# Performance work log

Hardware: AMD Instinct MI355X
Metric: run time of the kernel (lower is better)

## Reference

```python
import jax, jax.numpy as jnp
import numpy as np

N_ROW = 50000
N_COL = 50000
E = 600000
D = 128
NEG_SLOPE = 0.01  # torch LeakyReLU default


def _leaky(x):
    return jnp.where(x >= 0, x, NEG_SLOPE * x)


def _mlp(x, W1, b1, W2, b2):
    # (Linear -> LeakyReLU) x2, matching nn.Sequential in Conv_layer
    h = _leaky(x @ W1 + b1)
    return _leaky(h @ W2 + b2)


def setup_inputs() -> dict:
    key = jax.random.key(0)
    ks = jax.random.split(key, 16)
    inp = {
        "feat_row": jax.random.normal(ks[0], (N_ROW, D), jnp.float32),
        "feat_col": jax.random.normal(ks[1], (N_COL, D), jnp.float32),
        "src_c2r": jax.random.randint(ks[2], (E,), 0, N_COL, jnp.int32),
        "dst_c2r": jax.random.randint(ks[3], (E,), 0, N_ROW, jnp.int32),
        "w_c2r": jax.random.uniform(ks[4], (E,), jnp.float32),
        "src_r2c": jax.random.randint(ks[5], (E,), 0, N_ROW, jnp.int32),
        "dst_r2c": jax.random.randint(ks[6], (E,), 0, N_COL, jnp.int32),
        "w_r2c": jax.random.uniform(ks[7], (E,), jnp.float32),
        "W1_c2r": jax.random.normal(ks[8], (D, D), jnp.float32) / np.sqrt(D),
        "b1_c2r": jax.random.normal(ks[9], (D,), jnp.float32) * 0.01,
        "W2_c2r": jax.random.normal(ks[10], (D, D), jnp.float32) / np.sqrt(D),
        "b2_c2r": jax.random.normal(ks[11], (D,), jnp.float32) * 0.01,
        "W1_r2c": jax.random.normal(ks[12], (D, D), jnp.float32) / np.sqrt(D),
        "b1_r2c": jax.random.normal(ks[13], (D,), jnp.float32) * 0.01,
        "W2_r2c": jax.random.normal(ks[14], (D, D), jnp.float32) / np.sqrt(D),
        "b2_r2c": jax.random.normal(ks[15], (D,), jnp.float32) * 0.01,
        "eps_c2r": jnp.zeros((), jnp.float32),  # DGL GINConv init_eps=0
        "eps_r2c": jnp.zeros((), jnp.float32),
    }
    return inp


def reference(feat_row, feat_col, src_c2r, dst_c2r, w_c2r, src_r2c, dst_r2c, w_r2c,
              W1_c2r, b1_c2r, W2_c2r, b2_c2r, W1_r2c, b1_r2c, W2_r2c, b2_r2c,
              eps_c2r, eps_r2c):
    # col -> row GINConv (edge-weighted sum aggregation)
    msg = feat_col[src_c2r] * w_c2r[:, None]                       # [E, D]
    agg_row = jax.ops.segment_sum(msg, dst_c2r, num_segments=N_ROW)
    h_row = _mlp((1.0 + eps_c2r) * feat_row + agg_row, W1_c2r, b1_c2r, W2_c2r, b2_c2r)
    # row -> col GINConv using updated row features
    msg2 = h_row[src_r2c] * w_r2c[:, None]                         # [E, D]
    agg_col = jax.ops.segment_sum(msg2, dst_r2c, num_segments=N_COL)
    h_col = _mlp((1.0 + eps_r2c) * feat_col + agg_col, W1_r2c, b1_r2c, W2_r2c, b2_r2c)
    # residual (use_residual=True): add pre-conv embeddings
    return h_row + feat_row, h_col + feat_col
```

## Files before the change

kernel.cpp:

```cpp
#include <hip/hip_runtime.h>
#include <hip/hip_bf16.h>

#define NROW 50000
#define NCOL 50000
#define DDIM 128
#define CAP  32

typedef __bf16 bf16_t;
typedef __bf16 bf16x2 __attribute__((ext_vector_type(2)));
typedef __bf16 bf16x8 __attribute__((ext_vector_type(8)));
typedef float  f32x4  __attribute__((ext_vector_type(4)));

__device__ __forceinline__ float lrelu(float v) { return v >= 0.f ? v : 0.01f * v; }

__device__ __forceinline__ float ldf(const void* p, size_t i, bool f) {
    return f ? ((const float*)p)[i] : (float)((const bf16_t*)p)[i];
}

__device__ __forceinline__ bool dtf(const int* flags, int fi) {
    return (fi == -1) ? true : (fi == -2) ? false : (flags[fi] != 0);
}

struct TensorTab { const void* p[18]; int n[18]; };

__global__ __launch_bounds__(256) void detect_zero(TensorTab T, int* flags,
                                                   int* z, int zn)
{
    const int tid = threadIdx.x;
    if (blockIdx.x >= 18) {
        int i = (blockIdx.x - 18) * 256 + tid;
        if (i < zn) z[i] = 0;
        return;
    }
    __shared__ int vb, vf;
    const int t = blockIdx.x;
    if (tid == 0) { vb = 0; vf = 0; }
    __syncthreads();
    const int n = T.n[t];
    const bool isFloatArr = (t != 2 && t != 3 && t != 5 && t != 6) && n >= 2;
    if (isFloatArr) {
        int nw = n / 2;
        int wi = (int)(((long long)tid * nw) >> 8);
        unsigned w = ((const unsigned*)T.p[t])[wi];
        unsigned low = w & 0xffffu;
        if (low) {
            int e = (int)((low >> 7) & 0xffu);
            if (e >= 90 && e <= 141) atomicAdd(&vb, 1);
            else                     atomicAdd(&vf, 1);
        }
    }
    __syncthreads();
    if (tid == 0) flags[t] = (isFloatArr && vf > vb) ? 1 : 0;
}

__device__ __forceinline__ void fill_edges(
    int e, const int* __restrict__ dst, const int* __restrict__ srcArr,
    const void* __restrict__ wArr, int nE, int* __restrict__ counts,
    int2* __restrict__ slots2, int* __restrict__ ovCnt,
    int* __restrict__ ovList, bool fW)
{
    if (e >= nE) return;
    int d = dst[e];
    int pos = atomicAdd(&counts[d], 1);
    if (pos < CAP) {
        int2 pk;
        pk.x = srcArr[e];
        pk.y = __float_as_int(ldf(wArr, e, fW));
        slots2[(size_t)d * CAP + pos] = pk;
    } else {
        int k = atomicAdd(ovCnt, 1);
        ovList[k] = e;
    }
}

struct WPtrs { const void* W[4]; int fi[4]; };

__device__ __forceinline__ void prep_one(WPtrs P, const int* flags,
                                         __bf16* wfp, int slot)
{
    if (slot >= 4 * 2048) return;
    int m = slot >> 11, sIdx = slot & 2047;
    bool f = flags[P.fi[m]] != 0;
    int l = sIdx & 63, combo = sIdx >> 6;
    int ct = combo >> 2, kk = combo & 3;
    int col  = ct * 16 + (l & 15);
    int krow = kk * 32 + (l >> 4) * 8;
    bf16x8 v;
#pragma unroll
    for (int j = 0; j < 8; ++j)
        v[j] = (__bf16)ldf(P.W[m], (size_t)(krow + j) * DDIM + col, f);
    ((bf16x8*)wfp)[slot] = v;
}

__device__ __forceinline__ void convert_one(const void* __restrict__ feat,
                                            __bf16* __restrict__ cbuf,
                                            int i, int n8, bool f)
{
    if (i >= n8) return;
    bf16x8 v;
    if (f) {
        f32x4 a = ((const f32x4*)feat)[i * 2];
        f32x4 c = ((const f32x4*)feat)[i * 2 + 1];
#pragma unroll
        for (int j = 0; j < 4; ++j) { v[j] = (__bf16)a[j]; v[j + 4] = (__bf16)c[j]; }
    } else {
        v = ((const bf16x8*)feat)[i];
    }
    ((bf16x8*)cbuf)[i] = v;
}

__global__ __launch_bounds__(256) void prep_fill_i(
    WPtrs P, const int* __restrict__ flags, __bf16* __restrict__ wfp,
    const void* __restrict__ feat, __bf16* __restrict__ cbuf, int n8,
    int fiFeat, int cb, int eb, int K7,
    const int* __restrict__ f_dst, const int* __restrict__ f_src,
    const void* __restrict__ f_w, int f_nE, int* __restrict__ f_counts,
    int2* __restrict__ f_slots2, int* __restrict__ f_ovCnt,
    int* __restrict__ f_ovList, int f_fiW)
{
    const int g = blockIdx.x;
    const int tid = threadIdx.x;
    if (g >= K7) {
        prep_one(P, flags, wfp, (g - K7) * 256 + tid);
        return;
    }
    int grp = g / 7, rem = g % 7;
    if (rem < 4) {
        int b = grp * 4 + rem;
        if (b >= cb) return;
        convert_one(feat, cbuf, b * 256 + tid, n8, dtf(flags, fiFeat));
    } else {
        int b = grp * 3 + (rem - 4);
        if (b >= eb) return;
        fill_edges(b * 256 + tid, f_dst, f_src, f_w, f_nE, f_counts,
                   f_slots2, f_ovCnt, f_ovList, dtf(flags, f_fiW));
    }
}

template <bool RESIDUAL, bool HOUT>
__global__ __launch_bounds__(256) void mlp_fused(
    const __bf16* __restrict__ gsrc, const int* __restrict__ counts,
    const int2* __restrict__ slots2, const int* __restrict__ srcArr,
    const int* __restrict__ dstArr, const void* __restrict__ wArr,
    const int* __restrict__ ovList, const int* __restrict__ ovCount, int fiW,
    const void* __restrict__ feat, const void* __restrict__ b1,
    const void* __restrict__ b2, const void* __restrict__ epsp,
    float* __restrict__ out, int N, const int* __restrict__ flags,
    int fiFeat, int fiB1, int fiB2, int fiEps,
    const __bf16* __restrict__ pW1, const __bf16* __restrict__ pW2,
    __bf16* __restrict__ hout,
    int mlpBlocks, int fillBlocks,
    const int* __restrict__ f_dst, const int* __restrict__ f_src,
    const void* __restrict__ f_w, int f_nE, int* __restrict__ f_counts,
    int2* __restrict__ f_slots2, int* __restrict__ f_ovCnt,
    int* __restrict__ f_ovList, int f_fiW)
{
    __shared__ alignas(16) __bf16 At[16 * 136];
    __shared__ alignas(16) __bf16 H1[16 * 136];

    const int tid = threadIdx.x;
    int bid;
    if (f_dst) {
        int grp = (int)blockIdx.x / 7, rem = (int)blockIdx.x % 7;
        if (rem >= 4) {
            int b = grp * 3 + (rem - 4);
            if (b < fillBlocks)
                fill_edges(b * 256 + tid, f_dst, f_src, f_w, f_nE, f_counts,
                           f_slots2, f_ovCnt, f_ovList, dtf(flags, f_fiW));
            return;
        }
        bid = grp * 4 + rem;
        if (bid >= mlpBlocks) return;
    } else {
        bid = blockIdx.x;
        if (bid >= mlpBlocks) return;
    }

    const bool fF  = flags[fiFeat] != 0;
    const bool fB1 = flags[fiB1] != 0;
    const bool fB2 = flags[fiB2] != 0;
    const bool fE  = flags[fiEps] != 0;

    const int lane = tid & 63;
    const int wave = tid >> 6;
    const int quad = lane >> 4;
    const int r    = lane & 15;
    const int rowBase = bid * 16;
    const float eps1 = 1.f + ldf(epsp, 0, fE);

    {
        const bf16x2* fb = (const bf16x2*)gsrc;
        for (int j = 0; j < 4; ++j) {
            int lrow = wave * 4 + j;
            int row  = rowBase + lrow;
            bf16x2 o;
            if (row < N) {
                int cntRaw = counts[row];
                int cnt = cntRaw > CAP ? CAP : cntRaw;
                int sr = 0; float wv = 0.f;
                if (lane < cnt) {
                    int2 pk = slots2[(size_t)row * CAP + lane];
                    sr = pk.x;
                    wv = __int_as_float(pk.y);
                }
                float2 acc0 = {0.f, 0.f}, acc1 = {0.f, 0.f};
                int i = 0;
                for (; i + 4 <= cnt; i += 4) {
                    int   a0 = __shfl(sr, i),     a1 = __shfl(sr, i + 1);
                    int   a2 = __shfl(sr, i + 2), a3 = __shfl(sr, i + 3);
                    float w0 = __shfl(wv, i),     w1 = __shfl(wv, i + 1);
                    float w2 = __shfl(wv, i + 2), w3 = __shfl(wv, i + 3);
                    bf16x2 v0 = fb[(size_t)a0 * 64 + lane];
                    bf16x2 v1 = fb[(size_t)a1 * 64 + lane];
                    bf16x2 v2 = fb[(size_t)a2 * 64 + lane];
                    bf16x2 v3 = fb[(size_t)a3 * 64 + lane];
                    acc0.x += (float)v0[0] * w0; acc0.y += (float)v0[1] * w0;
                    acc1.x += (float)v1[0] * w1; acc1.y += (float)v1[1] * w1;
                    acc0.x += (float)v2[0] * w2; acc0.y += (float)v2[1] * w2;
                    acc1.x += (float)v3[0] * w3; acc1.y += (float)v3[1] * w3;
                }
                for (; i < cnt; ++i) {
                    int   a0 = __shfl(sr, i);
                    float w0 = __shfl(wv, i);
                    bf16x2 v0 = fb[(size_t)a0 * 64 + lane];
                    acc0.x += (float)v0[0] * w0; acc0.y += (float)v0[1] * w0;
                }
                if (cntRaw > CAP) {
                    const bool fW = dtf(flags, fiW);
                    int nOv = *ovCount;
                    for (int k = 0; k < nOv; ++k) {
                        int e = ovList[k];
                        if (dstArr[e] == row) {
                            int s = srcArr[e];
                            float wf = ldf(wArr, e, fW);
                            bf16x2 v = fb[(size_t)s * 64 + lane];
                            acc0.x += (float)v[0] * wf;
                            acc0.y += (float)v[1] * wf;
                        }
                    }
                }
                float ax = acc0.x + acc1.x, ay = acc0.y + acc1.y;
                float f0, f1;
                if (fF) {
                    float2 fv = ((const float2*)((const float*)feat +
                                 (size_t)row * DDIM))[lane];
                    f0 = fv.x; f1 = fv.y;
                } else {
                    bf16x2 fv = ((const bf16x2*)((const bf16_t*)feat +
                                 (size_t)row * DDIM))[lane];
                    f0 = (float)fv[0]; f1 = (float)fv[1];
                }
                o[0] = (__bf16)(f0 * eps1 + ax);
                o[1] = (__bf16)(f1 * eps1 + ay);
            } else {
                o[0] = (__bf16)0.f; o[1] = (__bf16)0.f;
            }
            *(bf16x2*)&At[lrow * 136 + lane * 2] = o;
        }
    }
    __syncthreads();

    bf16x8 a[4];
#pragma unroll
    for (int kk = 0; kk < 4; ++kk)
        a[kk] = *(const bf16x8*)&At[r * 136 + kk * 32 + quad * 8];

    const int ct0 = wave * 2, ct1 = ct0 + 1;

    const bf16x8* pw1v = (const bf16x8*)pW1;
    bf16x8 wfa[4], wfb[4];
#pragma unroll
    for (int kk = 0; kk < 4; ++kk) {
        wfa[kk] = pw1v[(ct0 * 4 + kk) * 64 + lane];
        wfb[kk] = pw1v[(ct1 * 4 + kk) * 64 + lane];
    }
    float b1a = ldf(b1, ct0 * 16 + r, fB1);
    float b1b = ldf(b1, ct1 * 16 + r, fB1);

    {
        f32x4 acc = {0.f, 0.f, 0.f, 0.f};
#pragma unroll
        for (int kk = 0; kk < 4; ++kk)
            acc = __builtin_amdgcn_mfma_f32_16x16x32_bf16(a[kk], wfa[kk], acc, 0, 0, 0);
#pragma unroll
        for (int gg = 0; gg < 4; ++gg)
            H1[(quad * 4 + gg) * 136 + ct0 * 16 + r] = (__bf16)lrelu(acc[gg] + b1a);
    }
    {
        f32x4 acc = {0.f, 0.f, 0.f, 0.f};
#pragma unroll
        for (int kk = 0; kk < 4; ++kk)
            acc = __builtin_amdgcn_mfma_f32_16x16x32_bf16(a[kk], wfb[kk], acc, 0, 0, 0);
#pragma unroll
        for (int gg = 0; gg < 4; ++gg)
            H1[(quad * 4 + gg) * 136 + ct1 * 16 + r] = (__bf16)lrelu(acc[gg] + b1b);
    }
    __syncthreads();

    bf16x8 a2[4];
#pragma unroll
    for (int kk = 0; kk < 4; ++kk)
        a2[kk] = *(const bf16x8*)&H1[r * 136 + kk * 32 + quad * 8];

    const bf16x8* pw2v = (const bf16x8*)pW2;
#pragma unroll
    for (int kk = 0; kk < 4; ++kk) {
        wfa[kk] = pw2v[(ct0 * 4 + kk) * 64 + lane];
        wfb[kk] = pw2v[(ct1 * 4 + kk) * 64 + lane];
    }
    float b2a = ldf(b2, ct0 * 16 + r, fB2);
    float b2b = ldf(b2, ct1 * 16 + r, fB2);

#pragma unroll
    for (int cp = 0; cp < 2; ++cp) {
        const int ct = cp ? ct1 : ct0;
        f32x4 acc = {0.f, 0.f, 0.f, 0.f};
#pragma unroll
        for (int kk = 0; kk < 4; ++kk)
            acc = __builtin_amdgcn_mfma_f32_16x16x32_bf16(
                a2[kk], cp ? wfb[kk] : wfa[kk], acc, 0, 0, 0);
        float bias = cp ? b2b : b2a;
#pragma unroll
        for (int gg = 0; gg < 4; ++gg) {
            int row = rowBase + quad * 4 + gg;
            float v = lrelu(acc[gg] + bias);
            if (HOUT)
                At[(quad * 4 + gg) * 136 + ct * 16 + r] = (__bf16)v;
            if (row < N) {
                int col = ct * 16 + r;
                if (RESIDUAL) v += ldf(feat, (size_t)row * DDIM + col, fF);
                out[(size_t)row * DDIM + col] = v;
            }
        }
    }

    if (HOUT) {
        __syncthreads();
        int row = tid >> 4;
        int k0  = (tid & 15) * 8;
        int g   = rowBase + row;
        if (g < N)
            *(bf16x8*)&hout[(size_t)g * DDIM + k0] =
                *(const bf16x8*)&At[row * 136 + k0];
    }
}

__global__ __launch_bounds__(256) void prep_fill(
    WPtrs P, const int* __restrict__ flags, __bf16* __restrict__ wfp,
    const void* __restrict__ feat, __bf16* __restrict__ cbuf, int n8,
    int fiFeat, int cblocks,
    const int* __restrict__ f_dst, const int* __restrict__ f_src,
    const void* __restrict__ f_w, int f_nE, int* __restrict__ f_counts,
    int2* __restrict__ f_slots2, int* __restrict__ f_ovCnt,
    int* __restrict__ f_ovList, int f_fiW)
{
    const int b = blockIdx.x;
    const int tid = threadIdx.x;
    if (b < cblocks) {
        convert_one(feat, cbuf, b * 256 + tid, n8, dtf(flags, fiFeat));
    } else if (b < cblocks + 32) {
        prep_one(P, flags, wfp, (b - cblocks) * 256 + tid);
    } else {
        int e = (b - cblocks - 32) * 256 + tid;
        fill_edges(e, f_dst, f_src, f_w, f_nE, f_counts, f_slots2,
                   f_ovCnt, f_ovList, dtf(flags, f_fiW));
    }
}

__global__ __launch_bounds__(256) void segsum_scan(
    const __bf16* __restrict__ gsrc, const int* __restrict__ counts,
    const int2* __restrict__ slots2, float* __restrict__ agg, int nRows,
    const int* __restrict__ srcArr, const int* __restrict__ dstArr,
    const void* __restrict__ wArr, const int* __restrict__ ovList,
    const int* __restrict__ ovCount, const int* __restrict__ flags, int fiW)
{
    int row = blockIdx.x * 4 + (threadIdx.x >> 6);
    if (row >= nRows) return;
    int lane = threadIdx.x & 63;

    int cntRaw = counts[row];
    int cnt = cntRaw > CAP ? CAP : cntRaw;

    int sr = 0; float wv = 0.f;
    if (lane < cnt) {
        int2 pk = slots2[(size_t)row * CAP + lane];
        sr = pk.x;
        wv = __int_as_float(pk.y);
    }

    float2* ap = (float2*)(agg + (size_t)row * DDIM) + lane;
    float2 acc0 = {0.f, 0.f}, acc1 = {0.f, 0.f};

    const bf16x2* fb = (const bf16x2*)gsrc;
    int i = 0;
    for (; i + 4 <= cnt; i += 4) {
        int   a0 = __shfl(sr, i),     a1 = __shfl(sr, i + 1);
        int   a2 = __shfl(sr, i + 2), a3 = __shfl(sr, i + 3);
        float w0 = __shfl(wv, i),     w1 = __shfl(wv, i + 1);
        float w2 = __shfl(wv, i + 2), w3 = __shfl(wv, i + 3);
        bf16x2 v0 = fb[(size_t)a0 * 64 + lane];
        bf16x2 v1 = fb[(size_t)a1 * 64 + lane];
        bf16x2 v2 = fb[(size_t)a2 * 64 + lane];
        bf16x2 v3 = fb[(size_t)a3 * 64 + lane];
        acc0.x += (float)v0[0] * w0; acc0.y += (float)v0[1] * w0;
        acc1.x += (float)v1[0] * w1; acc1.y += (float)v1[1] * w1;
        acc0.x += (float)v2[0] * w2; acc0.y += (float)v2[1] * w2;
        acc1.x += (float)v3[0] * w3; acc1.y += (float)v3[1] * w3;
    }
    for (; i < cnt; ++i) {
        int   a0 = __shfl(sr, i);
        float w0 = __shfl(wv, i);
        bf16x2 v0 = fb[(size_t)a0 * 64 + lane];
        acc0.x += (float)v0[0] * w0; acc0.y += (float)v0[1] * w0;
    }
    if (cntRaw > CAP) {
        const bool fW = dtf(flags, fiW);
        int nOv = *ovCount;
        for (int k = 0; k < nOv; ++k) {
            int e = ovList[k];
            if (dstArr[e] == row) {
                int s = srcArr[e];
                float wf = ldf(wArr, e, fW);
                bf16x2 v = fb[(size_t)s * 64 + lane];
                acc0.x += (float)v[0] * wf; acc0.y += (float)v[1] * wf;
            }
        }
    }
    acc0.x += acc1.x; acc0.y += acc1.y;
    *ap = acc0;
}

template <bool RESIDUAL, bool HOUT>
__global__ __launch_bounds__(256) void mlp_cs(
    const void* __restrict__ feat, const float* __restrict__ agg,
    const void* __restrict__ b1, const void* __restrict__ b2,
    const void* __restrict__ epsp, float* __restrict__ out, int N,
    const int* __restrict__ flags, int fiFeat, int fiB1, int fiB2, int fiEps,
    const __bf16* __restrict__ pW1, const __bf16* __restrict__ pW2,
    __bf16* __restrict__ hout,
    int mblocks,
    const int* __restrict__ f_dst, const int* __restrict__ f_src,
    const void* __restrict__ f_w, int f_nE, int* __restrict__ f_counts,
    int2* __restrict__ f_slots2, int* __restrict__ f_ovCnt,
    int* __restrict__ f_ovList, int f_fiW)
{
    __shared__ alignas(16) __bf16 At[16 * 136];
    __shared__ alignas(16) __bf16 H1[16 * 136];

    const int tid = threadIdx.x;
    if (f_dst && (int)blockIdx.x >= mblocks) {
        int e = ((int)blockIdx.x - mblocks) * 256 + tid;
        fill_edges(e, f_dst, f_src, f_w, f_nE, f_counts, f_slots2,
                   f_ovCnt, f_ovList, dtf(flags, f_fiW));
        return;
    }

    const bool fF  = flags[fiFeat] != 0;
    const bool fB1 = flags[fiB1] != 0;
    const bool fB2 = flags[fiB2] != 0;
    const bool fE  = flags[fiEps] != 0;

    const int lane = tid & 63;
    const int wave = tid >> 6;
    const int quad = lane >> 4;
    const int r    = lane & 15;
    const int rowBase = blockIdx.x * 16;
    const float eps1 = 1.f + ldf(epsp, 0, fE);

    {
        int row = tid >> 4;
        int k0  = (tid & 15) * 8;
        int g   = rowBase + row;
        bf16x8 av;
        if (g < N) {
            size_t base = (size_t)g * DDIM + k0;
            const f32x4* gp = (const f32x4*)(agg + base);
            f32x4 g0 = gp[0], g1 = gp[1];
            if (fF) {
                const f32x4* fp = (const f32x4*)((const float*)feat + base);
                f32x4 f0 = fp[0], f1 = fp[1];
#pragma unroll
                for (int j = 0; j < 4; ++j) {
                    av[j]     = (__bf16)(f0[j] * eps1 + g0[j]);
                    av[j + 4] = (__bf16)(f1[j] * eps1 + g1[j]);
                }
            } else {
                bf16x8 fv = *(const bf16x8*)((const bf16_t*)feat + base);
#pragma unroll
                for (int j = 0; j < 4; ++j) {
                    av[j]     = (__bf16)((float)fv[j]     * eps1 + g0[j]);
                    av[j + 4] = (__bf16)((float)fv[j + 4] * eps1 + g1[j]);
                }
            }
        } else {
#pragma unroll
            for (int j = 0; j < 8; ++j) av[j] = (__bf16)0.f;
        }
        *(bf16x8*)&At[row * 136 + k0] = av;
    }
    __syncthreads();

    bf16x8 a[4];
#pragma unroll
    for (int kk = 0; kk < 4; ++kk)
        a[kk] = *(const bf16x8*)&At[r * 136 + kk * 32 + quad * 8];

    const int ct0 = wave * 2, ct1 = ct0 + 1;

    const bf16x8* pw1v = (const bf16x8*)pW1;
    bf16x8 wfa[4], wfb[4];
#pragma unroll
    for (int kk = 0; kk < 4; ++kk) {
        wfa[kk] = pw1v[(ct0 * 4 + kk) * 64 + lane];
        wfb[kk] = pw1v[(ct1 * 4 + kk) * 64 + lane];
    }
    float b1a = ldf(b1, ct0 * 16 + r, fB1);
    float b1b = ldf(b1, ct1 * 16 + r, fB1);

    {
        f32x4 acc = {0.f, 0.f, 0.f, 0.f};
#pragma unroll
        for (int kk = 0; kk < 4; ++kk)
            acc = __builtin_amdgcn_mfma_f32_16x16x32_bf16(a[kk], wfa[kk], acc, 0, 0, 0);
#pragma unroll
        for (int gg = 0; gg < 4; ++gg)
            H1[(quad * 4 + gg) * 136 + ct0 * 16 + r] = (__bf16)lrelu(acc[gg] + b1a);
    }
    {
        f32x4 acc = {0.f, 0.f, 0.f, 0.f};
#pragma unroll
        for (int kk = 0; kk < 4; ++kk)
            acc = __builtin_amdgcn_mfma_f32_16x16x32_bf16(a[kk], wfb[kk], acc, 0, 0, 0);
#pragma unroll
        for (int gg = 0; gg < 4; ++gg)
            H1[(quad * 4 + gg) * 136 + ct1 * 16 + r] = (__bf16)lrelu(acc[gg] + b1b);
    }
    __syncthreads();

    bf16x8 a2[4];
#pragma unroll
    for (int kk = 0; kk < 4; ++kk)
        a2[kk] = *(const bf16x8*)&H1[r * 136 + kk * 32 + quad * 8];

    const bf16x8* pw2v = (const bf16x8*)pW2;
#pragma unroll
    for (int kk = 0; kk < 4; ++kk) {
        wfa[kk] = pw2v[(ct0 * 4 + kk) * 64 + lane];
        wfb[kk] = pw2v[(ct1 * 4 + kk) * 64 + lane];
    }
    float b2a = ldf(b2, ct0 * 16 + r, fB2);
    float b2b = ldf(b2, ct1 * 16 + r, fB2);

#pragma unroll
    for (int cp = 0; cp < 2; ++cp) {
        const int ct = cp ? ct1 : ct0;
        f32x4 acc = {0.f, 0.f, 0.f, 0.f};
#pragma unroll
        for (int kk = 0; kk < 4; ++kk)
            acc = __builtin_amdgcn_mfma_f32_16x16x32_bf16(
                a2[kk], cp ? wfb[kk] : wfa[kk], acc, 0, 0, 0);
        float bias = cp ? b2b : b2a;
#pragma unroll
        for (int gg = 0; gg < 4; ++gg) {
            int row = rowBase + quad * 4 + gg;
            float v = lrelu(acc[gg] + bias);
            if (HOUT)
                At[(quad * 4 + gg) * 136 + ct * 16 + r] = (__bf16)v;
            if (row < N) {
                int col = ct * 16 + r;
                if (RESIDUAL) v += ldf(feat, (size_t)row * DDIM + col, fF);
                out[(size_t)row * DDIM + col] = v;
            }
        }
    }

    if (HOUT) {
        __syncthreads();
        int row = tid >> 4;
        int k0  = (tid & 15) * 8;
        int g   = rowBase + row;
        if (g < N)
            *(bf16x8*)&hout[(size_t)g * DDIM + k0] =
                *(const bf16x8*)&At[row * 136 + k0];
    }
}

__global__ __launch_bounds__(256) void scatter_any(
    const void* __restrict__ feat, const int* __restrict__ src,
    const int* __restrict__ dst, const void* __restrict__ w,
    float* __restrict__ agg, int nE,
    const int* __restrict__ flags, int fiFeat, int fiW)
{
    const bool fF = dtf(flags, fiFeat);
    const bool fW = dtf(flags, fiW);
    int g = blockIdx.x * 256 + threadIdx.x;
    int e = g >> 5;
    if (e >= nE) return;
    int c = (g & 31) << 2;
    int s = src[e], d = dst[e];
    float wf = ldf(w, e, fW);
    size_t base = (size_t)s * DDIM + c;
    float* ap = agg + (size_t)d * DDIM + c;
    unsafeAtomicAdd(ap + 0, ldf(feat, base + 0, fF) * wf);
    unsafeAtomicAdd(ap + 1, ldf(feat, base + 1, fF) * wf);
    unsafeAtomicAdd(ap + 2, ldf(feat, base + 2, fF) * wf);
    unsafeAtomicAdd(ap + 3, ldf(feat, base + 3, fF) * wf);
}

__global__ __launch_bounds__(256) void residual_add(
    float* __restrict__ out, const void* __restrict__ feat, int n4,
    const int* __restrict__ flags, int fiFeat)
{
    const bool fF = flags[fiFeat] != 0;
    int i = blockIdx.x * 256 + threadIdx.x;
    if (i >= n4) return;
    f32x4 o = ((const f32x4*)out)[i];
    f32x4 r;
#pragma unroll
    for (int j = 0; j < 4; ++j) r[j] = o[j] + ldf(feat, (size_t)i * 4 + j, fF);
    ((f32x4*)out)[i] = r;
}

__device__ __forceinline__ void fill_wfrag(const void* __restrict__ W, bool f,
                                           __bf16* wf, int tid)
{
#pragma unroll
    for (int i = 0; i < 8; ++i) {
        int sIdx  = tid + i * 256;
        int l     = sIdx & 63;
        int combo = sIdx >> 6;
        int ct = combo >> 2, kk = combo & 3;
        int col  = ct * 16 + (l & 15);
        int krow = kk * 32 + (l >> 4) * 8;
        __bf16* dp = wf + (size_t)sIdx * 8;
#pragma unroll
        for (int j = 0; j < 8; ++j)
            dp[j] = (__bf16)ldf(W, (size_t)(krow + j) * DDIM + col, f);
    }
}

template <bool RESIDUAL>
__global__ __launch_bounds__(256) void mlp_kernel(
    const void* __restrict__ feat, const float* __restrict__ agg,
    const void* __restrict__ W1, const void* __restrict__ b1,
    const void* __restrict__ W2, const void* __restrict__ b2,
    const void* __restrict__ epsp, float* __restrict__ out, int N,
    const int* __restrict__ flags,
    int fiFeat, int fiW1, int fiB1, int fiW2, int fiB2, int fiEps)
{
    __shared__ alignas(16) __bf16 wf[32 * 64 * 8];
    __shared__ alignas(16) __bf16 h1t[64 * 136];

    const bool fF  = flags[fiFeat] != 0;
    const bool fB1 = flags[fiB1] != 0;
    const bool fB2 = flags[fiB2] != 0;
    const bool fE  = flags[fiEps] != 0;

    const int tid  = threadIdx.x;
    const int lane = tid & 63;
    const int wave = tid >> 6;
    const int quad = lane >> 4;
    const int r    = lane & 15;

    fill_wfrag(W1, flags[fiW1] != 0, wf, tid);

    const float eps1 = 1.f + ldf(epsp, 0, fE);
    const int rowBase = blockIdx.x * 64 + wave * 16;

    bf16x8 a[4];
    {
        int rowA = rowBase + r;
        if (rowA < N) {
            size_t fb = (size_t)rowA * DDIM + quad * 8;
            const f32x4* gp = (const f32x4*)(agg + fb);
            if (fF) {
                const f32x4* fp = (const f32x4*)((const float*)feat + fb);
#pragma unroll
                for (int kk = 0; kk < 4; ++kk) {
                    f32x4 f0 = fp[kk * 8], f1 = fp[kk * 8 + 1];
                    f32x4 g0 = gp[kk * 8], g1 = gp[kk * 8 + 1];
                    bf16x8 av;
#pragma unroll
                    for (int j = 0; j < 4; ++j) {
                        av[j]     = (__bf16)(f0[j] * eps1 + g0[j]);
                        av[j + 4] = (__bf16)(f1[j] * eps1 + g1[j]);
                    }
                    a[kk] = av;
                }
            } else {
                const bf16x8* fp = (const bf16x8*)((const bf16_t*)feat + fb);
#pragma unroll
                for (int kk = 0; kk < 4; ++kk) {
                    bf16x8 fv = fp[kk * 4];
                    f32x4 g0 = gp[kk * 8], g1 = gp[kk * 8 + 1];
                    bf16x8 av;
#pragma unroll
                    for (int j = 0; j < 4; ++j) {
                        av[j]     = (__bf16)((float)fv[j]     * eps1 + g0[j]);
                        av[j + 4] = (__bf16)((float)fv[j + 4] * eps1 + g1[j]);
                    }
                    a[kk] = av;
                }
            }
        } else {
#pragma unroll
            for (int kk = 0; kk < 4; ++kk)
#pragma unroll
                for (int j = 0; j < 8; ++j) a[kk][j] = (__bf16)0.f;
        }
    }

    __syncthreads();

    const bf16x8* wv = (const bf16x8*)wf;
#pragma unroll
    for (int ct = 0; ct < 8; ++ct) {
        f32x4 acc = {0.f, 0.f, 0.f, 0.f};
#pragma unroll
        for (int kk = 0; kk < 4; ++kk)
            acc = __builtin_amdgcn_mfma_f32_16x16x32_bf16(
                a[kk], wv[(ct * 4 + kk) * 64 + lane], acc, 0, 0, 0);
        float bias = ldf(b1, ct * 16 + r, fB1);
#pragma unroll
        for (int gg = 0; gg < 4; ++gg)
            h1t[(wave * 16 + quad * 4 + gg) * 136 + ct * 16 + r] =
                (__bf16)lrelu(acc[gg] + bias);
    }
    __syncthreads();

    bf16x8 a2[4];
#pragma unroll
    for (int kk = 0; kk < 4; ++kk)
        a2[kk] = *(const bf16x8*)&h1t[(wave * 16 + r) * 136 + kk * 32 + quad * 8];

    fill_wfrag(W2, flags[fiW2] != 0, wf, tid);
    __syncthreads();

#pragma unroll
    for (int ct = 0; ct < 8; ++ct) {
        f32x4 acc = {0.f, 0.f, 0.f, 0.f};
#pragma unroll
        for (int kk = 0; kk < 4; ++kk)
            acc = __builtin_amdgcn_mfma_f32_16x16x32_bf16(
                a2[kk], wv[(ct * 4 + kk) * 64 + lane], acc, 0, 0, 0);
        float bias = ldf(b2, ct * 16 + r, fB2);
#pragma unroll
        for (int gg = 0; gg < 4; ++gg) {
            int row = rowBase + quad * 4 + gg;
            if (row < N) {
                int col = ct * 16 + r;
                float v = lrelu(acc[gg] + bias);
                if (RESIDUAL) v += ldf(feat, (size_t)row * DDIM + col, fF);
                out[(size_t)row * DDIM + col] = v;
            }
        }
    }
}

extern "C" void kernel_launch(void* const* d_in, const int* in_sizes, int n_in,
                              void* d_out, int out_size, void* d_ws, size_t ws_size,
                              hipStream_t stream)
{
    const int* src_c2r = (const int*)d_in[2];
    const int* dst_c2r = (const int*)d_in[3];
    const int* src_r2c = (const int*)d_in[5];
    const int* dst_r2c = (const int*)d_in[6];
    const int nE = in_sizes[2];

    char* wsb = (char*)d_ws;
    int*    flags  = (int*)wsb;
    __bf16* wfprep = (__bf16*)(wsb + 128);

    int*    cntA   = (int*)(wsb + 128 + 131072);
    int*    ovCntA = cntA + NROW;
    int*    cntB   = cntA + NROW + 8;
    int*    ovCntB = cntA + 2 * NROW + 8;
    size_t  o3 = 128 + 131072 + ((size_t)2 * NROW + 16) * 4;
    o3 = (o3 + 15) & ~(size_t)15;
    int2*   sl2A = (int2*)(wsb + o3);  o3 += (size_t)NROW * CAP * 8;
    int2*   sl2B = (int2*)(wsb + o3);  o3 += (size_t)NROW * CAP * 8;
    int*    ovLA = (int*)(wsb + o3);   o3 += (size_t)nE * 4;
    int*    ovLB = (int*)(wsb + o3);   o3 += (size_t)nE * 4;
    o3 = (o3 + 15) & ~(size_t)15;
    __bf16* cbX  = (__bf16*)(wsb + o3); o3 += (size_t)NCOL * DDIM * 2;
    __bf16* cbH  = (__bf16*)(wsb + o3); o3 += (size_t)NROW * DDIM * 2;
    const size_t NEED_A3 = o3;

    size_t  ofsA2   = 128 + 131072 + ((size_t)2 * NROW + 16) * 4;
    ofsA2 = (ofsA2 + 15) & ~(size_t)15;
    int2*   slots2A2  = (int2*)(wsb + ofsA2);
    size_t  ofsOvA2   = ofsA2 + (size_t)NROW * CAP * 8;
    int*    ovListA2  = (int*)(wsb + ofsOvA2);
    int*    ovListB2  = ovListA2 + nE;
    size_t  ofsCbA2   = (ofsOvA2 + (size_t)nE * 8 + 15) & ~(size_t)15;
    __bf16* cbufA2    = (__bf16*)(wsb + ofsCbA2);
    const size_t NEED_A2 = ofsCbA2 + (size_t)NROW * DDIM * 2;

    const bool tierA3 = ws_size >= NEED_A3;
    const bool tierA2 = ws_size >= NEED_A2;

    TensorTab T;
    for (int i = 0; i < 18; ++i) { T.p[i] = d_in[i]; T.n[i] = in_sizes[i]; }

    float* out_row = (float*)d_out;
    float* out_col = out_row + (size_t)NROW * DDIM;
    const size_t aggBytes = (size_t)NROW * DDIM * sizeof(float);

    const int eblocks  = (nE + 255) / 256;
    const int sblocks  = (nE * 32 + 255) / 256;
    const int mblocksR = (NROW + 63) / 64;
    const int mblocksC = (NCOL + 63) / 64;
    const int csR      = (NROW + 15) / 16;
    const int csC      = (NCOL + 15) / 16;
    const int gblocksR = (NROW + 3) / 4;
    const int gblocksC = (NCOL + 3) / 4;
    const int cblocks  = (NCOL * DDIM / 8 + 255) / 256;
    const int zn2      = 2 * NROW + 16;
    const int zb2      = (zn2 + 255) / 256;

    WPtrs P;
    P.W[0] = d_in[8];  P.fi[0] = 8;
    P.W[1] = d_in[10]; P.fi[1] = 10;
    P.W[2] = d_in[12]; P.fi[2] = 12;
    P.W[3] = d_in[14]; P.fi[3] = 14;

    if (tierA3) {
        detect_zero<<<18 + zb2, 256, 0, stream>>>(T, flags, cntA, zn2);
        {
            int ka = (cblocks + 3) / 4, kb = (eblocks + 2) / 3;
            int K = ka > kb ? ka : kb;
            prep_fill_i<<<7 * K + 32, 256, 0, stream>>>(
                P, flags, wfprep, d_in[1], cbX, NCOL * DDIM / 8, 1,
                cblocks, eblocks, 7 * K,
                dst_c2r, src_c2r, d_in[4], nE, cntA, sl2A, ovCntA, ovLA, 4);
        }
        {
            int ka = (csR + 3) / 4, kb = (eblocks + 2) / 3;
            int K = ka > kb ? ka : kb;
            mlp_fused<true, true><<<7 * K, 256, 0, stream>>>(
                cbX, cntA, sl2A, src_c2r, dst_c2r, d_in[4], ovLA, ovCntA, 4,
                d_in[0], d_in[9], d_in[11], d_in[16],
                out_row, NROW, flags, 0, 9, 11, 16,
                wfprep + 0 * 16384, wfprep + 1 * 16384, cbH,
                csR, eblocks, dst_r2c, src_r2c, d_in[7], nE, cntB, sl2B,
                ovCntB, ovLB, 7);
        }
        mlp_fused<true, false><<<csC, 256, 0, stream>>>(
            cbH, cntB, sl2B, src_r2c, dst_r2c, d_in[7], ovLB, ovCntB, 7,
            d_in[1], d_in[13], d_in[15], d_in[17],
            out_col, NCOL, flags, 1, 13, 15, 17,
            wfprep + 2 * 16384, wfprep + 3 * 16384, nullptr,
            csC, 0, nullptr, nullptr, nullptr, 0, nullptr, nullptr,
            nullptr, nullptr, 0);
    } else if (tierA2) {
        detect_zero<<<18 + zb2, 256, 0, stream>>>(T, flags, cntA, zn2);
        prep_fill<<<cblocks + 32 + eblocks, 256, 0, stream>>>(
            P, flags, wfprep, d_in[1], cbufA2, NCOL * DDIM / 8, 1, cblocks,
            dst_c2r, src_c2r, d_in[4], nE, cntA, slots2A2, ovCntA,
            ovListA2, 4);
        segsum_scan<<<gblocksR, 256, 0, stream>>>(cbufA2, cntA, slots2A2,
            out_col, NROW, src_c2r, dst_c2r, d_in[4], ovListA2, ovCntA,
            flags, 4);
        mlp_cs<true, true><<<csR + eblocks, 256, 0, stream>>>(
            d_in[0], out_col, d_in[9], d_in[11], d_in[16],
            out_row, NROW, flags, 0, 9, 11, 16,
            wfprep + 0 * 16384, wfprep + 1 * 16384, cbufA2,
            csR, dst_r2c, src_r2c, d_in[7], nE, cntB, slots2A2,
            ovCntB, ovListB2, 7);
        segsum_scan<<<gblocksC, 256, 0, stream>>>(cbufA2, cntB, slots2A2,
            out_col, NCOL, src_r2c, dst_r2c, d_in[7], ovListB2, ovCntB,
            flags, 7);
        mlp_cs<true, false><<<csC, 256, 0, stream>>>(
            d_in[1], out_col, d_in[13], d_in[15], d_in[17],
            out_col, NCOL, flags, 1, 13, 15, 17,
            wfprep + 2 * 16384, wfprep + 3 * 16384, nullptr,
            csC, nullptr, nullptr, nullptr, 0, nullptr, nullptr,
            nullptr, nullptr, 0);
    } else {
        detect_zero<<<18, 256, 0, stream>>>(T, flags, nullptr, 0);
        hipMemsetAsync(out_col, 0, aggBytes, stream);
        scatter_any<<<sblocks, 256, 0, stream>>>(d_in[1], src_c2r, dst_c2r,
            d_in[4], out_col, nE, flags, 1, 4);
        mlp_kernel<false><<<mblocksR, 256, 0, stream>>>(
            d_in[0], out_col, d_in[8], d_in[9], d_in[10], d_in[11], d_in[16],
            out_row, NROW, flags, 0, 8, 9, 10, 11, 16);

        hipMemsetAsync(out_col, 0, aggBytes, stream);
        scatter_any<<<sblocks, 256, 0, stream>>>(out_row, src_r2c, dst_r2c,
            d_in[7], out_col, nE, flags, -1, 7);
        residual_add<<<(NROW * DDIM / 4 + 255) / 256, 256, 0, stream>>>(
            out_row, d_in[0], NROW * DDIM / 4, flags, 0);
        mlp_kernel<true><<<mblocksC, 256, 0, stream>>>(
            d_in[1], out_col, d_in[12], d_in[13], d_in[14], d_in[15], d_in[17],
            out_col, NCOL, flags, 1, 12, 13, 14, 15, 17);
    }
}
```

Measured before the change: 306.6 us.

## Store edge ids in slot buckets and use 1024-thread blocks, one row per wave

Bucket slots now hold only the edge id (4 bytes) instead of a packed src/weight pair (8 bytes), halving slot-table traffic during the fill. The gather stage then does an extra indirect load of src and weight per edge. Kernels move to 1024-thread blocks where each of 16 waves aggregates one row, and only 8 waves run the MFMA stages. This raises gather parallelism per block but leaves half the waves idle during the MLP and may lower occupancy.

```diff
diff --git a/kernel.cpp b/kernel.cpp
--- a/kernel.cpp
+++ b/kernel.cpp
@@ -53,6 +53,21 @@
     if (tid == 0) flags[t] = (isFloatArr && vf > vb) ? 1 : 0;
 }
 
+__device__ __forceinline__ void fill_edges_id(
+    int e, const int* __restrict__ dst, int nE, int* __restrict__ counts,
+    int* __restrict__ slots, int* __restrict__ ovCnt, int* __restrict__ ovList)
+{
+    if (e >= nE) return;
+    int d = dst[e];
+    int pos = atomicAdd(&counts[d], 1);
+    if (pos < CAP) {
+        slots[(size_t)d * CAP + pos] = e;
+    } else {
+        int k = atomicAdd(ovCnt, 1);
+        ovList[k] = e;
+    }
+}
+
 __device__ __forceinline__ void fill_edges(
     int e, const int* __restrict__ dst, const int* __restrict__ srcArr,
     const void* __restrict__ wArr, int nE, int* __restrict__ counts,
@@ -109,38 +124,37 @@
     ((bf16x8*)cbuf)[i] = v;
 }
 
-__global__ __launch_bounds__(256) void prep_fill_i(
+__global__ __launch_bounds__(1024) void prep_fill_i2(
     WPtrs P, const int* __restrict__ flags, __bf16* __restrict__ wfp,
     const void* __restrict__ feat, __bf16* __restrict__ cbuf, int n8,
     int fiFeat, int cb, int eb, int K7,
-    const int* __restrict__ f_dst, const int* __restrict__ f_src,
-    const void* __restrict__ f_w, int f_nE, int* __restrict__ f_counts,
-    int2* __restrict__ f_slots2, int* __restrict__ f_ovCnt,
-    int* __restrict__ f_ovList, int f_fiW)
+    const int* __restrict__ f_dst, int f_nE, int* __restrict__ f_counts,
+    int* __restrict__ f_slots, int* __restrict__ f_ovCnt,
+    int* __restrict__ f_ovList)
 {
     const int g = blockIdx.x;
     const int tid = threadIdx.x;
     if (g >= K7) {
-        prep_one(P, flags, wfp, (g - K7) * 256 + tid);
+        prep_one(P, flags, wfp, (g - K7) * 1024 + tid);
         return;
     }
     int grp = g / 7, rem = g % 7;
     if (rem < 4) {
         int b = grp * 4 + rem;
         if (b >= cb) return;
-        convert_one(feat, cbuf, b * 256 + tid, n8, dtf(flags, fiFeat));
+        convert_one(feat, cbuf, b * 1024 + tid, n8, dtf(flags, fiFeat));
     } else {
         int b = grp * 3 + (rem - 4);
         if (b >= eb) return;
-        fill_edges(b * 256 + tid, f_dst, f_src, f_w, f_nE, f_counts,
-                   f_slots2, f_ovCnt, f_ovList, dtf(flags, f_fiW));
+        fill_edges_id(b * 1024 + tid, f_dst, f_nE, f_counts, f_slots,
+                      f_ovCnt, f_ovList);
     }
 }
 
 template <bool RESIDUAL, bool HOUT>
-__global__ __launch_bounds__(256) void mlp_fused(
+__global__ __launch_bounds__(1024) void mlp_fused2(
     const __bf16* __restrict__ gsrc, const int* __restrict__ counts,
-    const int2* __restrict__ slots2, const int* __restrict__ srcArr,
+    const int* __restrict__ slots, const int* __restrict__ srcArr,
     const int* __restrict__ dstArr, const void* __restrict__ wArr,
     const int* __restrict__ ovList, const int* __restrict__ ovCount, int fiW,
     const void* __restrict__ feat, const void* __restrict__ b1,
@@ -150,10 +164,9 @@
     const __bf16* __restrict__ pW1, const __bf16* __restrict__ pW2,
     __bf16* __restrict__ hout,
     int mlpBlocks, int fillBlocks,
-    const int* __restrict__ f_dst, const int* __restrict__ f_src,
-    const void* __restrict__ f_w, int f_nE, int* __restrict__ f_counts,
-    int2* __restrict__ f_slots2, int* __restrict__ f_ovCnt,
-    int* __restrict__ f_ovList, int f_fiW)
+    const int* __restrict__ f_dst, int f_nE, int* __restrict__ f_counts,
+    int* __restrict__ f_slots, int* __restrict__ f_ovCnt,
+    int* __restrict__ f_ovList)
 {
     __shared__ alignas(16) __bf16 At[16 * 136];
     __shared__ alignas(16) __bf16 H1[16 * 136];
@@ -165,8 +178,8 @@
         if (rem >= 4) {
             int b = grp * 3 + (rem - 4);
             if (b < fillBlocks)
-                fill_edges(b * 256 + tid, f_dst, f_src, f_w, f_nE, f_counts,
-                           f_slots2, f_ovCnt, f_ovList, dtf(flags, f_fiW));
+                fill_edges_id(b * 1024 + tid, f_dst, f_nE, f_counts,
+                              f_slots, f_ovCnt, f_ovList);
             return;
         }
         bid = grp * 4 + rem;
@@ -180,6 +193,7 @@
     const bool fB1 = flags[fiB1] != 0;
     const bool fB2 = flags[fiB2] != 0;
     const bool fE  = flags[fiEps] != 0;
+    const bool fW  = dtf(flags, fiW);
 
     const int lane = tid & 63;
     const int wave = tid >> 6;
@@ -190,140 +204,113 @@
 
     {
         const bf16x2* fb = (const bf16x2*)gsrc;
-        for (int j = 0; j < 4; ++j) {
-            int lrow = wave * 4 + j;
-            int row  = rowBase + lrow;
-            bf16x2 o;
-            if (row < N) {
-                int cntRaw = counts[row];
-                int cnt = cntRaw > CAP ? CAP : cntRaw;
-                int sr = 0; float wv = 0.f;
-                if (lane < cnt) {
-                    int2 pk = slots2[(size_t)row * CAP + lane];
-                    sr = pk.x;
-                    wv = __int_as_float(pk.y);
-                }
-                float2 acc0 = {0.f, 0.f}, acc1 = {0.f, 0.f};
-                int i = 0;
-                for (; i + 4 <= cnt; i += 4) {
-                    int   a0 = __shfl(sr, i),     a1 = __shfl(sr, i + 1);
-                    int   a2 = __shfl(sr, i + 2), a3 = __shfl(sr, i + 3);
-                    float w0 = __shfl(wv, i),     w1 = __shfl(wv, i + 1);
-                    float w2 = __shfl(wv, i + 2), w3 = __shfl(wv, i + 3);
-                    bf16x2 v0 = fb[(size_t)a0 * 64 + lane];
-                    bf16x2 v1 = fb[(size_t)a1 * 64 + lane];
-                    bf16x2 v2 = fb[(size_t)a2 * 64 + lane];
-                    bf16x2 v3 = fb[(size_t)a3 * 64 + lane];
-                    acc0.x += (float)v0[0] * w0; acc0.y += (float)v0[1] * w0;
-                    acc1.x += (float)v1[0] * w1; acc1.y += (float)v1[1] * w1;
-                    acc0.x += (float)v2[0] * w2; acc0.y += (float)v2[1] * w2;
-                    acc1.x += (float)v3[0] * w3; acc1.y += (float)v3[1] * w3;
-                }
-                for (; i < cnt; ++i) {
-                    int   a0 = __shfl(sr, i);
-                    float w0 = __shfl(wv, i);
-                    bf16x2 v0 = fb[(size_t)a0 * 64 + lane];
-                    acc0.x += (float)v0[0] * w0; acc0.y += (float)v0[1] * w0;
-                }
-                if (cntRaw > CAP) {
-                    const bool fW = dtf(flags, fiW);
-                    int nOv = *ovCount;
-                    for (int k = 0; k < nOv; ++k) {
-                        int e = ovList[k];
-                        if (dstArr[e] == row) {
-                            int s = srcArr[e];
-                            float wf = ldf(wArr, e, fW);
-                            bf16x2 v = fb[(size_t)s * 64 + lane];
-                            acc0.x += (float)v[0] * wf;
-                            acc0.y += (float)v[1] * wf;
-                        }
+        int row = rowBase + wave;
+        bf16x2 o;
+        if (row < N) {
+            int cntRaw = counts[row];
+            int cnt = cntRaw > CAP ? CAP : cntRaw;
+            int sr = 0; float wv = 0.f;
+            if (lane < cnt) {
+                int e = slots[(size_t)row * CAP + lane];
+                sr = srcArr[e];
+                wv = ldf(wArr, e, fW);
+            }
+            float2 acc0 = {0.f, 0.f}, acc1 = {0.f, 0.f};
+            int i = 0;
+            for (; i + 4 <= cnt; i += 4) {
+                int   a0 = __shfl(sr, i),     a1 = __shfl(sr, i + 1);
+                int   a2 = __shfl(sr, i + 2), a3 = __shfl(sr, i + 3);
+                float w0 = __shfl(wv, i),     w1 = __shfl(wv, i + 1);
+                float w2 = __shfl(wv, i + 2), w3 = __shfl(wv, i + 3);
+                bf16x2 v0 = fb[(size_t)a0 * 64 + lane];
+                bf16x2 v1 = fb[(size_t)a1 * 64 + lane];
+                bf16x2 v2 = fb[(size_t)a2 * 64 + lane];
+                bf16x2 v3 = fb[(size_t)a3 * 64 + lane];
+                acc0.x += (float)v0[0] * w0; acc0.y += (float)v0[1] * w0;
+                acc1.x += (float)v1[0] * w1; acc1.y += (float)v1[1] * w1;
+                acc0.x += (float)v2[0] * w2; acc0.y += (float)v2[1] * w2;
+                acc1.x += (float)v3[0] * w3; acc1.y += (float)v3[1] * w3;
+            }
+            for (; i < cnt; ++i) {
+                int   a0 = __shfl(sr, i);
+                float w0 = __shfl(wv, i);
+                bf16x2 v0 = fb[(size_t)a0 * 64 + lane];
+                acc0.x += (float)v0[0] * w0; acc0.y += (float)v0[1] * w0;
+            }
+            if (cntRaw > CAP) {
+                int nOv = *ovCount;
+                for (int k = 0; k < nOv; ++k) {
+                    int e = ovList[k];
+                    if (dstArr[e] == row) {
+                        int s = srcArr[e];
+                        float wf = ldf(wArr, e, fW);
+                        bf16x2 v = fb[(size_t)s * 64 + lane];
+                        acc0.x += (float)v[0] * wf;
+                        acc0.y += (float)v[1] * wf;
                     }
                 }
-                float ax = acc0.x + acc1.x, ay = acc0.y + acc1.y;
-                float f0, f1;
-                if (fF) {
-                    float2 fv = ((const float2*)((const float*)feat +
-                                 (size_t)row * DDIM))[lane];
-                    f0 = fv.x; f1 = fv.y;
-                } else {
-                    bf16x2 fv = ((const bf16x2*)((const bf16_t*)feat +
-                                 (size_t)row * DDIM))[lane];
-                    f0 = (float)fv[0]; f1 = (float)fv[1];
-                }
-                o[0] = (__bf16)(f0 * eps1 + ax);
-                o[1] = (__bf16)(f1 * eps1 + ay);
+            }
+            float ax = acc0.x + acc1.x, ay = acc0.y + acc1.y;
+            float f0, f1;
+            if (fF) {
+                float2 fv = ((const float2*)((const float*)feat +
+                             (size_t)row * DDIM))[lane];
+                f0 = fv.x; f1 = fv.y;
             } else {
-                o[0] = (__bf16)0.f; o[1] = (__bf16)0.f;
-            }
-            *(bf16x2*)&At[lrow * 136 + lane * 2] = o;
-        }
+                bf16x2 fv = ((const bf16x2*)((const bf16_t*)feat +
+                             (size_t)row * DDIM))[lane];
+                f0 = (float)fv[0]; f1 = (float)fv[1];
+            }
+            o[0] = (__bf16)(f0 * eps1 + ax);
+            o[1] = (__bf16)(f1 * eps1 + ay);
+        } else {
+            o[0] = (__bf16)0.f; o[1] = (__bf16)0.f;
+        }
+        *(bf16x2*)&At[wave * 136 + lane * 2] = o;
     }
     __syncthreads();
 
-    bf16x8 a[4];
-#pragma unroll
-    for (int kk = 0; kk < 4; ++kk)
-        a[kk] = *(const bf16x8*)&At[r * 136 + kk * 32 + quad * 8];
-
-    const int ct0 = wave * 2, ct1 = ct0 + 1;
-
-    const bf16x8* pw1v = (const bf16x8*)pW1;
-    bf16x8 wfa[4], wfb[4];
-#pragma unroll
-    for (int kk = 0; kk < 4; ++kk) {
-        wfa[kk] = pw1v[(ct0 * 4 + kk) * 64 + lane];
-        wfb[kk] = pw1v[(ct1 * 4 + kk) * 64 + lane];
-    }
-    float b1a = ldf(b1, ct0 * 16 + r, fB1);
-    float b1b = ldf(b1, ct1 * 16 + r, fB1);
-
-    {
+    const int ct = wave;
+    if (wave < 8) {
+        bf16x8 a[4];
+#pragma unroll
+        for (int kk = 0; kk < 4; ++kk)
+            a[kk] = *(const bf16x8*)&At[r * 136 + kk * 32 + quad * 8];
+        const bf16x8* pw1v = (const bf16x8*)pW1;
+        bf16x8 w1f[4];
+#pragma unroll
+        for (int kk = 0; kk < 4; ++kk)
+            w1f[kk] = pw1v[(ct * 4 + kk) * 64 + lane];
+        float b1v = ldf(b1, ct * 16 + r, fB1);
         f32x4 acc = {0.f, 0.f, 0.f, 0.f};
 #pragma unroll
         for (int kk = 0; kk < 4; ++kk)
-            acc = __builtin_amdgcn_mfma_f32_16x16x32_bf16(a[kk], wfa[kk], acc, 0, 0, 0);
+            acc = __builtin_amdgcn_mfma_f32_16x16x32_bf16(a[kk], w1f[kk], acc, 0, 0, 0);
 #pragma unroll
         for (int gg = 0; gg < 4; ++gg)
-            H1[(quad * 4 + gg) * 136 + ct0 * 16 + r] = (__bf16)lrelu(acc[gg] + b1a);
-    }
-    {
+            H1[(quad * 4 + gg) * 136 + ct * 16 + r] = (__bf16)lrelu(acc[gg] + b1v);
+    }
+    __syncthreads();
+
+    if (wave < 8) {
+        bf16x8 a2[4];
+#pragma unroll
+        for (int kk = 0; kk < 4; ++kk)
+            a2[kk] = *(const bf16x8*)&H1[r * 136 + kk * 32 + quad * 8];
+        const bf16x8* pw2v = (const bf16x8*)pW2;
+        bf16x8 w2f[4];
+#pragma unroll
+        for (int kk = 0; kk < 4; ++kk)
+            w2f[kk] = pw2v[(ct * 4 + kk) * 64 + lane];
+        float b2v = ldf(b2, ct * 16 + r, fB2);
         f32x4 acc = {0.f, 0.f, 0.f, 0.f};
 #pragma unroll
         for (int kk = 0; kk < 4; ++kk)
-            acc = __builtin_amdgcn_mfma_f32_16x16x32_bf16(a[kk], wfb[kk], acc, 0, 0, 0);
-#pragma unroll
-        for (int gg = 0; gg < 4; ++gg)
-            H1[(quad * 4 + gg) * 136 + ct1 * 16 + r] = (__bf16)lrelu(acc[gg] + b1b);
-    }
-    __syncthreads();
-
-    bf16x8 a2[4];
-#pragma unroll
-    for (int kk = 0; kk < 4; ++kk)
-        a2[kk] = *(const bf16x8*)&H1[r * 136 + kk * 32 + quad * 8];
-
-    const bf16x8* pw2v = (const bf16x8*)pW2;
-#pragma unroll
-    for (int kk = 0; kk < 4; ++kk) {
-        wfa[kk] = pw2v[(ct0 * 4 + kk) * 64 + lane];
-        wfb[kk] = pw2v[(ct1 * 4 + kk) * 64 + lane];
-    }
-    float b2a = ldf(b2, ct0 * 16 + r, fB2);
-    float b2b = ldf(b2, ct1 * 16 + r, fB2);
-
-#pragma unroll
-    for (int cp = 0; cp < 2; ++cp) {
-        const int ct = cp ? ct1 : ct0;
-        f32x4 acc = {0.f, 0.f, 0.f, 0.f};
-#pragma unroll
-        for (int kk = 0; kk < 4; ++kk)
-            acc = __builtin_amdgcn_mfma_f32_16x16x32_bf16(
-                a2[kk], cp ? wfb[kk] : wfa[kk], acc, 0, 0, 0);
-        float bias = cp ? b2b : b2a;
+            acc = __builtin_amdgcn_mfma_f32_16x16x32_bf16(a2[kk], w2f[kk], acc, 0, 0, 0);
 #pragma unroll
         for (int gg = 0; gg < 4; ++gg) {
             int row = rowBase + quad * 4 + gg;
-            float v = lrelu(acc[gg] + bias);
+            float v = lrelu(acc[gg] + b2v);
             if (HOUT)
                 At[(quad * 4 + gg) * 136 + ct * 16 + r] = (__bf16)v;
             if (row < N) {
@@ -336,12 +323,14 @@
 
     if (HOUT) {
         __syncthreads();
-        int row = tid >> 4;
-        int k0  = (tid & 15) * 8;
-        int g   = rowBase + row;
-        if (g < N)
-            *(bf16x8*)&hout[(size_t)g * DDIM + k0] =
-                *(const bf16x8*)&At[row * 136 + k0];
+        if (tid < 256) {
+            int row = tid >> 4;
+            int k0  = (tid & 15) * 8;
+            int g   = rowBase + row;
+            if (g < N)
+                *(bf16x8*)&hout[(size_t)g * DDIM + k0] =
+                    *(const bf16x8*)&At[row * 136 + k0];
+        }
     }
 }
 
@@ -775,16 +764,16 @@
     int*    ovCntA = cntA + NROW;
     int*    cntB   = cntA + NROW + 8;
     int*    ovCntB = cntA + 2 * NROW + 8;
-    size_t  o3 = 128 + 131072 + ((size_t)2 * NROW + 16) * 4;
-    o3 = (o3 + 15) & ~(size_t)15;
-    int2*   sl2A = (int2*)(wsb + o3);  o3 += (size_t)NROW * CAP * 8;
-    int2*   sl2B = (int2*)(wsb + o3);  o3 += (size_t)NROW * CAP * 8;
-    int*    ovLA = (int*)(wsb + o3);   o3 += (size_t)nE * 4;
-    int*    ovLB = (int*)(wsb + o3);   o3 += (size_t)nE * 4;
-    o3 = (o3 + 15) & ~(size_t)15;
-    __bf16* cbX  = (__bf16*)(wsb + o3); o3 += (size_t)NCOL * DDIM * 2;
-    __bf16* cbH  = (__bf16*)(wsb + o3); o3 += (size_t)NROW * DDIM * 2;
-    const size_t NEED_A3 = o3;
+    size_t  o4 = 128 + 131072 + ((size_t)2 * NROW + 16) * 4;
+    o4 = (o4 + 15) & ~(size_t)15;
+    int*    slotsA = (int*)(wsb + o4);  o4 += (size_t)NROW * CAP * 4;
+    int*    slotsB = (int*)(wsb + o4);  o4 += (size_t)NROW * CAP * 4;
+    int*    ovLA   = (int*)(wsb + o4);  o4 += (size_t)nE * 4;
+    int*    ovLB   = (int*)(wsb + o4);  o4 += (size_t)nE * 4;
+    o4 = (o4 + 15) & ~(size_t)15;
+    __bf16* cbX  = (__bf16*)(wsb + o4); o4 += (size_t)NCOL * DDIM * 2;
+    __bf16* cbH  = (__bf16*)(wsb + o4); o4 += (size_t)NROW * DDIM * 2;
+    const size_t NEED_A4 = o4;
 
     size_t  ofsA2   = 128 + 131072 + ((size_t)2 * NROW + 16) * 4;
     ofsA2 = (ofsA2 + 15) & ~(size_t)15;
@@ -796,7 +785,7 @@
     __bf16* cbufA2    = (__bf16*)(wsb + ofsCbA2);
     const size_t NEED_A2 = ofsCbA2 + (size_t)NROW * DDIM * 2;
 
-    const bool tierA3 = ws_size >= NEED_A3;
+    const bool tierA4 = ws_size >= NEED_A4;
     const bool tierA2 = ws_size >= NEED_A2;
 
     TensorTab T;
@@ -824,34 +813,34 @@
     P.W[2] = d_in[12]; P.fi[2] = 12;
     P.W[3] = d_in[14]; P.fi[3] = 14;
 
-    if (tierA3) {
+    if (tierA4) {
+        const int n8  = NCOL * DDIM / 8;
+        const int cb4 = (n8 + 1023) / 1024;
+        const int eb4 = (nE + 1023) / 1024;
         detect_zero<<<18 + zb2, 256, 0, stream>>>(T, flags, cntA, zn2);
         {
-            int ka = (cblocks + 3) / 4, kb = (eblocks + 2) / 3;
+            int ka = (cb4 + 3) / 4, kb = (eb4 + 2) / 3;
             int K = ka > kb ? ka : kb;
-            prep_fill_i<<<7 * K + 32, 256, 0, stream>>>(
-                P, flags, wfprep, d_in[1], cbX, NCOL * DDIM / 8, 1,
-                cblocks, eblocks, 7 * K,
-                dst_c2r, src_c2r, d_in[4], nE, cntA, sl2A, ovCntA, ovLA, 4);
+            prep_fill_i2<<<7 * K + 8, 1024, 0, stream>>>(
+                P, flags, wfprep, d_in[1], cbX, n8, 1, cb4, eb4, 7 * K,
+                dst_c2r, nE, cntA, slotsA, ovCntA, ovLA);
         }
         {
-            int ka = (csR + 3) / 4, kb = (eblocks + 2) / 3;
+            int ka = (csR + 3) / 4, kb = (eb4 + 2) / 3;
             int K = ka > kb ? ka : kb;
-            mlp_fused<true, true><<<7 * K, 256, 0, stream>>>(
-                cbX, cntA, sl2A, src_c2r, dst_c2r, d_in[4], ovLA, ovCntA, 4,
+            mlp_fused2<true, true><<<7 * K, 1024, 0, stream>>>(
+                cbX, cntA, slotsA, src_c2r, dst_c2r, d_in[4], ovLA, ovCntA, 4,
                 d_in[0], d_in[9], d_in[11], d_in[16],
                 out_row, NROW, flags, 0, 9, 11, 16,
                 wfprep + 0 * 16384, wfprep + 1 * 16384, cbH,
-                csR, eblocks, dst_r2c, src_r2c, d_in[7], nE, cntB, sl2B,
-                ovCntB, ovLB, 7);
-        }
-        mlp_fused<true, false><<<csC, 256, 0, stream>>>(
-            cbH, cntB, sl2B, src_r2c, dst_r2c, d_in[7], ovLB, ovCntB, 7,
+                csR, eb4, dst_r2c, nE, cntB, slotsB, ovCntB, ovLB);
+        }
+        mlp_fused2<true, false><<<csC, 1024, 0, stream>>>(
+            cbH, cntB, slotsB, src_r2c, dst_r2c, d_in[7], ovLB, ovCntB, 7,
             d_in[1], d_in[13], d_in[15], d_in[17],
             out_col, NCOL, flags, 1, 13, 15, 17,
             wfprep + 2 * 16384, wfprep + 3 * 16384, nullptr,
-            csC, 0, nullptr, nullptr, nullptr, 0, nullptr, nullptr,
-            nullptr, nullptr, 0);
+            csC, 0, nullptr, 0, nullptr, nullptr, nullptr, nullptr);
     } else if (tierA2) {
         detect_zero<<<18 + zb2, 256, 0, stream>>>(T, flags, cntA, zn2);
         prep_fill<<<cblocks + 32 + eblocks, 256, 0, stream>>>(
```

Result: slower. 320.4 us (+4.5%).
